# Optimization experiments

Measured on AMD Instinct MI355X. Metric: run time of the kernel, lower is better.

## Reference

```python
import jax, jax.numpy as jnp
import numpy as np

D_MODEL = 1024
NUM_HEADS = 16
DEPTH = D_MODEL // NUM_HEADS


def setup_inputs() -> dict:
    key = jax.random.key(0)
    ks = jax.random.split(key, 9)
    B, S = 2, 2048
    s = 1.0 / np.sqrt(D_MODEL)
    inp = {
        "inputs": jax.random.normal(ks[0], (B, S, D_MODEL), dtype=jnp.float32),
        "wq": jax.random.normal(ks[1], (D_MODEL, D_MODEL), dtype=jnp.float32) * s,
        "bq": jnp.zeros((D_MODEL,), dtype=jnp.float32),
        "wk": jax.random.normal(ks[2], (D_MODEL, D_MODEL), dtype=jnp.float32) * s,
        "bk": jnp.zeros((D_MODEL,), dtype=jnp.float32),
        "wv": jax.random.normal(ks[3], (D_MODEL, D_MODEL), dtype=jnp.float32) * s,
        "bv": jnp.zeros((D_MODEL,), dtype=jnp.float32),
        "wo": jax.random.normal(ks[4], (D_MODEL, D_MODEL), dtype=jnp.float32) * s,
        "bo": jnp.zeros((D_MODEL,), dtype=jnp.float32),
    }
    return inp


def _split_heads(x, B):
    # [B, S, D] -> [B, H, S, depth]
    S = x.shape[1]
    return x.reshape(B, S, NUM_HEADS, DEPTH).transpose(0, 2, 1, 3)


def reference(inputs, wq, bq, wk, bk, wv, bv, wo, bo):
    B, S, _ = inputs.shape
    q = _split_heads(inputs @ wq + bq, B)  # [B,H,S,d]
    k = _split_heads(inputs @ wk + bk, B)
    v = _split_heads(inputs @ wv + bv, B)
    scale = 1.0 / jnp.sqrt(jnp.asarray(DEPTH, dtype=inputs.dtype))
    logits = jnp.einsum("bhqd,bhkd->bhqk", q, k) * scale  # [B,H,S,S]
    attn = jax.nn.softmax(logits, axis=-1)
    out = jnp.einsum("bhqk,bhkd->bhqd", attn, v)  # [B,H,S,d]
    out = out.transpose(0, 2, 1, 3).reshape(B, S, D_MODEL)
    return out @ wo + bo
```

## Files before the change

kernel.cpp:

```cpp
#include <hip/hip_runtime.h>
#include <math.h>

#define SEQ     2048
#define DM      1024
#define NH      16
#define DEPTH   64
#define MTOT    4096

typedef __attribute__((ext_vector_type(8))) _Float16 f16x8;
typedef __attribute__((ext_vector_type(2))) __fp16   fp16v2;
typedef __attribute__((ext_vector_type(4))) float    f32x4;
typedef __attribute__((ext_vector_type(2))) unsigned u32x2;

static __device__ inline unsigned pkh(float a, float b) {
    union { fp16v2 h; unsigned u; } c;
    c.h = __builtin_amdgcn_cvt_pkrtz(a, b);
    return c.u;
}

#define GLOBAL_AS(p) ((const __attribute__((address_space(1))) void*)(p))
#define LDS_AS(p)    ((__attribute__((address_space(3))) void*)(p))

#define K2  0.18033688011112043f
#define C2 -17.31234049066756f
#define EXP2(x) __builtin_amdgcn_exp2f(x)

#define DMA_SRC_C8(lane)  ((((lane) & 3) ^ (((lane) >> 3) & 3)) * 8)
#define FRAG_C8(lx,quad)  ((((quad) ^ (((lx) >> 1) & 3))) * 8)
#define DMA_SRC64(lane)   ((((lane) & 7) ^ (((lane) >> 3) & 7)) * 8)
#define FRAG64(lx,c)      ((((c) ^ ((lx) & 7))) * 8)

__global__ __launch_bounds__(256)
void prep(const float* __restrict__ X,
          const float* __restrict__ w0, const float* __restrict__ w1,
          const float* __restrict__ w2, const float* __restrict__ w3,
          short* __restrict__ Xb,
          short* __restrict__ o0, short* __restrict__ o1,
          short* __restrict__ o2, short* __restrict__ o3) {
    const int t = threadIdx.x;
    const int z = blockIdx.z;
    if (z >= 4) {
        int r0 = (z - 4) * 1024 + blockIdx.x * 64;
        int c0 = blockIdx.y * 64;
        #pragma unroll
        for (int i = 0; i < 4; i++) {
            int row = r0 + i * 16 + (t >> 4);
            int c4  = c0 + (t & 15) * 4;
            float4 v = *(const float4*)&X[(size_t)row * DM + c4];
            u32x2 o; o.x = pkh(v.x, v.y); o.y = pkh(v.z, v.w);
            *(u32x2*)&Xb[(size_t)row * DM + c4] = o;
        }
        return;
    }
    const float* W; short* O;
    switch (z) {
        case 0: W = w0; O = o0; break;
        case 1: W = w1; O = o1; break;
        case 2: W = w2; O = o2; break;
        default: W = w3; O = o3; break;
    }
    __shared__ float Tf[64][65];
    const int k0 = blockIdx.x * 64, n0 = blockIdx.y * 64;
    #pragma unroll
    for (int i = 0; i < 4; i++) {
        int row = i * 16 + (t >> 4);
        int c4  = (t & 15) * 4;
        float4 v = *(const float4*)&W[(size_t)(k0 + row) * DM + n0 + c4];
        Tf[row][c4 + 0] = v.x; Tf[row][c4 + 1] = v.y;
        Tf[row][c4 + 2] = v.z; Tf[row][c4 + 3] = v.w;
    }
    __syncthreads();
    #pragma unroll
    for (int i = 0; i < 4; i++) {
        int nrow = i * 16 + (t >> 4);
        int kc4  = (t & 15) * 4;
        u32x2 o;
        o.x = pkh(Tf[kc4 + 0][nrow], Tf[kc4 + 1][nrow]);
        o.y = pkh(Tf[kc4 + 2][nrow], Tf[kc4 + 3][nrow]);
        *(u32x2*)&O[(size_t)(n0 + nrow) * DM + k0 + kc4] = o;
    }
}

__global__ __launch_bounds__(256)
void gemm_qkv(const short* __restrict__ Xb,
              const short* __restrict__ Wqt, const short* __restrict__ Wkt,
              const short* __restrict__ Wvt,
              const float* __restrict__ bq, const float* __restrict__ bk,
              const float* __restrict__ bv,
              short* __restrict__ Qw, short* __restrict__ Kw,
              short* __restrict__ Vtw) {
    const int z = blockIdx.z;
    const short* A; const short* B; const float* bias;
    if (z == 0)      { A = Xb;  B = Wqt; bias = bq; }
    else if (z == 1) { A = Xb;  B = Wkt; bias = bk; }
    else             { A = Wvt; B = Xb;  bias = bv; }
    const int bx = blockIdx.x;
    int m0, n0;
    if (z < 2) { n0 = (bx & 7) * 128; m0 = (bx >> 3) * 128; }
    else       { m0 = (bx & 7) * 128; n0 = (bx >> 3) * 128; }

    __shared__ short As[128 * 64];
    __shared__ short Bs[128 * 64];
    const int t = threadIdx.x, lane = t & 63, w = t >> 6;
    const int lx = lane & 15, quad = lane >> 4;
    const int wm = (w & 1) * 64, wn = (w >> 1) * 64;
    const int r8 = lane >> 3;
    const int cs = DMA_SRC64(lane);

    f32x4 acc[4][4];
    #pragma unroll
    for (int i = 0; i < 4; i++)
        #pragma unroll
        for (int j = 0; j < 4; j++)
            acc[i][j] = (f32x4){0.f, 0.f, 0.f, 0.f};

    for (int k0 = 0; k0 < DM; k0 += 64) {
        #pragma unroll
        for (int j = 0; j < 4; j++) {
            int rb = w * 32 + j * 8;
            __builtin_amdgcn_global_load_lds(
                GLOBAL_AS(A + (size_t)(m0 + rb + r8) * DM + k0 + cs),
                LDS_AS(As + rb * 64), 16, 0, 0);
            __builtin_amdgcn_global_load_lds(
                GLOBAL_AS(B + (size_t)(n0 + rb + r8) * DM + k0 + cs),
                LDS_AS(Bs + rb * 64), 16, 0, 0);
        }
        __syncthreads();

        #pragma unroll
        for (int ks = 0; ks < 2; ks++) {
            const int fo = FRAG64(lx, ks * 4 + quad);
            f16x8 af[4], bfr[4];
            #pragma unroll
            for (int mt = 0; mt < 4; mt++)
                af[mt] = *(f16x8*)&As[(wm + mt * 16 + lx) * 64 + fo];
            #pragma unroll
            for (int nt = 0; nt < 4; nt++)
                bfr[nt] = *(f16x8*)&Bs[(wn + nt * 16 + lx) * 64 + fo];
            #pragma unroll
            for (int mt = 0; mt < 4; mt++)
                #pragma unroll
                for (int nt = 0; nt < 4; nt++)
                    acc[mt][nt] = __builtin_amdgcn_mfma_f32_16x16x32_f16(
                        af[mt], bfr[nt], acc[mt][nt], 0, 0, 0);
        }
        __syncthreads();
    }

    if (z < 2) {
        short* Cp = (z == 0) ? Qw : Kw;
        float bi[4];
        #pragma unroll
        for (int nt = 0; nt < 4; nt++) bi[nt] = bias[n0 + wn + nt * 16 + lx];
        #pragma unroll
        for (int mt = 0; mt < 4; mt++) {
            #pragma unroll
            for (int reg = 0; reg < 4; reg++) {
                int row = m0 + wm + mt * 16 + quad * 4 + reg;
                u32x2 o;
                o.x = pkh(acc[mt][0][reg] + bi[0], acc[mt][1][reg] + bi[1]);
                o.y = pkh(acc[mt][2][reg] + bi[2], acc[mt][3][reg] + bi[3]);
                *(u32x2*)&Cp[(size_t)row * DM + n0 + wn + 4 * lx] = o;
            }
        }
    } else {
        int colbase = n0 + wn;
        int bsel    = colbase >> 11;
        int kb      = colbase & 2047;
        short* Vbh  = Vtw + (size_t)bsel * ((size_t)NH * DEPTH * SEQ);
        int so = ((lx >> 2) * 8) + ((lx & 3) * 2);
        #pragma unroll
        for (int mt = 0; mt < 4; mt++) {
            #pragma unroll
            for (int reg = 0; reg < 4; reg++) {
                int row = m0 + wm + mt * 16 + quad * 4 + reg;
                float bb = bias[row];
                unsigned w01 = pkh(acc[mt][0][reg] + bb, acc[mt][1][reg] + bb);
                unsigned w23 = pkh(acc[mt][2][reg] + bb, acc[mt][3][reg] + bb);
                *(unsigned*)&Vbh[(size_t)row * SEQ + kb + so]      = w01;
                *(unsigned*)&Vbh[(size_t)row * SEQ + kb + so + 32] = w23;
            }
        }
    }
}

__global__ __launch_bounds__(256)
void gemm_out(const short* __restrict__ A, const short* __restrict__ B,
              const float* __restrict__ bias, float* __restrict__ C) {
    __shared__ short As[128 * 64];
    __shared__ short Bs[64 * 64];
    const int t = threadIdx.x, lane = t & 63, w = t >> 6;
    const int lx = lane & 15, quad = lane >> 4;
    const int n0 = blockIdx.x * 64, m0 = blockIdx.y * 128;
    const int wm = (w & 1) * 64, wn = (w >> 1) * 32;
    const int r8 = lane >> 3;
    const int cs = DMA_SRC64(lane);

    f32x4 acc[4][2];
    #pragma unroll
    for (int i = 0; i < 4; i++)
        #pragma unroll
        for (int j = 0; j < 2; j++)
            acc[i][j] = (f32x4){0.f, 0.f, 0.f, 0.f};

    for (int k0 = 0; k0 < DM; k0 += 64) {
        #pragma unroll
        for (int j = 0; j < 4; j++) {
            int rb = w * 32 + j * 8;
            __builtin_amdgcn_global_load_lds(
                GLOBAL_AS(A + (size_t)(m0 + rb + r8) * DM + k0 + cs),
                LDS_AS(As + rb * 64), 16, 0, 0);
        }
        #pragma unroll
        for (int j = 0; j < 2; j++) {
            int rb = w * 16 + j * 8;
            __builtin_amdgcn_global_load_lds(
                GLOBAL_AS(B + (size_t)(n0 + rb + r8) * DM + k0 + cs),
                LDS_AS(Bs + rb * 64), 16, 0, 0);
        }
        __syncthreads();

        #pragma unroll
        for (int ks = 0; ks < 2; ks++) {
            const int fo = FRAG64(lx, ks * 4 + quad);
            f16x8 af[4], bfr[2];
            #pragma unroll
            for (int mt = 0; mt < 4; mt++)
                af[mt] = *(f16x8*)&As[(wm + mt * 16 + lx) * 64 + fo];
            #pragma unroll
            for (int nt = 0; nt < 2; nt++)
                bfr[nt] = *(f16x8*)&Bs[(wn + nt * 16 + lx) * 64 + fo];
            #pragma unroll
            for (int mt = 0; mt < 4; mt++)
                #pragma unroll
                for (int nt = 0; nt < 2; nt++)
                    acc[mt][nt] = __builtin_amdgcn_mfma_f32_16x16x32_f16(
                        af[mt], bfr[nt], acc[mt][nt], 0, 0, 0);
        }
        __syncthreads();
    }

    #pragma unroll
    for (int mt = 0; mt < 4; mt++)
        #pragma unroll
        for (int nt = 0; nt < 2; nt++)
            #pragma unroll
            for (int reg = 0; reg < 4; reg++) {
                int row = m0 + wm + mt * 16 + quad * 4 + reg;
                int col = n0 + wn + nt * 16 + lx;
                C[(size_t)row * DM + col] = acc[mt][nt][reg] + bias[col];
            }
}

__global__ __launch_bounds__(512)
void flash_mfma(const short* __restrict__ Q, const short* __restrict__ K,
                const short* __restrict__ Vt, short* __restrict__ O) {
    __shared__ short Ks[2][2][128 * 32];
    __shared__ short Vs[2][4][64 * 32];

    const int t = threadIdx.x, lane = t & 63, w = t >> 6;
    const int lx = lane & 15, quad = lane >> 4;
    const int h = blockIdx.y, bb = blockIdx.z;
    const int q0 = blockIdx.x * 128;
    const int r4 = lane >> 2;
    const int cs  = DMA_SRC_C8(lane);
    const int fa  = FRAG_C8(lx, quad);

    f16x8 qa[2];
    #pragma unroll
    for (int ks = 0; ks < 2; ks++)
        qa[ks] = *(const f16x8*)&Q[(size_t)(bb * SEQ + q0 + w * 16 + lx) * DM
                                   + h * DEPTH + ks * 32 + quad * 8];

    f32x4 of[4];
    float l_acc = 0.f;
    #pragma unroll
    for (int dt = 0; dt < 4; dt++) of[dt] = (f32x4){0.f, 0.f, 0.f, 0.f};

    const short* Kb = K  + (size_t)bb * SEQ * DM + h * DEPTH;
    const short* Vb = Vt + (size_t)(bb * NH + h) * DEPTH * SEQ;

    const int kdh = w >> 2;
    const int krg = (w & 3) * 16;
    const int vsh = w & 3;
    const int vdg = (w >> 2) * 16;

    auto stage = [&](int kt, int sb) {
        const int kbase = kt * 128;
        const short* kg = Kb + (size_t)(kbase + krg + r4) * DM + kdh * 32;
        __builtin_amdgcn_global_load_lds(GLOBAL_AS(kg + cs),
            LDS_AS(&Ks[sb][kdh][krg * 32]), 16, 0, 0);
        __builtin_amdgcn_global_load_lds(GLOBAL_AS(kg + (size_t)64 * DM + cs),
            LDS_AS(&Ks[sb][kdh][(krg + 64) * 32]), 16, 0, 0);
        const short* vg = Vb + (size_t)(vdg + r4) * SEQ + kbase + vsh * 32;
        __builtin_amdgcn_global_load_lds(GLOBAL_AS(vg + cs),
            LDS_AS(&Vs[sb][vsh][vdg * 32]), 16, 0, 0);
        __builtin_amdgcn_global_load_lds(GLOBAL_AS(vg + (size_t)32 * SEQ + cs),
            LDS_AS(&Vs[sb][vsh][(vdg + 32) * 32]), 16, 0, 0);
    };

    stage(0, 0);
    __syncthreads();

    int buf = 0;
    for (int kt = 0; kt < SEQ / 128; kt++) {
        if (kt + 1 < SEQ / 128) stage(kt + 1, buf ^ 1);

        f32x4 st[8];
        #pragma unroll
        for (int nt = 0; nt < 8; nt++)
            st[nt] = (f32x4){0.f, 0.f, 0.f, 0.f};
        #pragma unroll
        for (int ks = 0; ks < 2; ks++) {
            #pragma unroll
            for (int g = 0; g < 2; g++) {
                f16x8 kb[4];
                #pragma unroll
                for (int n4 = 0; n4 < 4; n4++)
                    kb[n4] = *(f16x8*)&Ks[buf][ks][((g * 4 + n4) * 16 + lx) * 32 + fa];
                __builtin_amdgcn_s_setprio(1);
                #pragma unroll
                for (int n4 = 0; n4 < 4; n4++)
                    st[g * 4 + n4] = __builtin_amdgcn_mfma_f32_16x16x32_f16(
                        kb[n4], qa[ks], st[g * 4 + n4], 0, 0, 0);
                __builtin_amdgcn_s_setprio(0);
            }
        }

        f16x8 pa[4];
        #pragma unroll
        for (int g = 0; g < 2; g++)
            #pragma unroll
            for (int ks = 0; ks < 2; ks++) {
                union { f16x8 v; unsigned u[4]; } pu;
                #pragma unroll
                for (int wd = 0; wd < 4; wd++) {
                    float pe = EXP2(fmaf(st[g * 4 + 2 * ks + 0][wd], K2, C2));
                    float po = EXP2(fmaf(st[g * 4 + 2 * ks + 1][wd], K2, C2));
                    l_acc += pe + po;
                    pu.u[wd] = pkh(pe, po);
                }
                pa[g * 2 + ks] = pu.v;
            }

        #pragma unroll
        for (int sh = 0; sh < 4; sh++) {
            f16x8 vb[4];
            #pragma unroll
            for (int dt = 0; dt < 4; dt++)
                vb[dt] = *(f16x8*)&Vs[buf][sh][(dt * 16 + lx) * 32 + fa];
            __builtin_amdgcn_s_setprio(1);
            #pragma unroll
            for (int dt = 0; dt < 4; dt++)
                of[dt] = __builtin_amdgcn_mfma_f32_16x16x32_f16(
                    pa[sh], vb[dt], of[dt], 0, 0, 0);
            __builtin_amdgcn_s_setprio(0);
        }

        __syncthreads();
        buf ^= 1;
    }

    _Float16* Oh = (_Float16*)O;
    {
        float l = l_acc;
        l += __shfl_xor(l, 16);
        l += __shfl_xor(l, 32);
        #pragma unroll
        for (int reg = 0; reg < 4; reg++) {
            float lrow = __shfl(l, quad * 4 + reg, 64);
            float inv  = 1.0f / lrow;
            size_t row = (size_t)bb * SEQ + q0 + w * 16 + quad * 4 + reg;
            #pragma unroll
            for (int dt = 0; dt < 4; dt++)
                Oh[row * DM + h * DEPTH + dt * 16 + lx] = (_Float16)(of[dt][reg] * inv);
        }
    }
}

extern "C" void kernel_launch(void* const* d_in, const int* in_sizes, int n_in,
                              void* d_out, int out_size, void* d_ws, size_t ws_size,
                              hipStream_t stream) {
    const float* X  = (const float*)d_in[0];
    const float* wq = (const float*)d_in[1];
    const float* bq = (const float*)d_in[2];
    const float* wk = (const float*)d_in[3];
    const float* bk = (const float*)d_in[4];
    const float* wv = (const float*)d_in[5];
    const float* bv = (const float*)d_in[6];
    const float* wo = (const float*)d_in[7];
    const float* bo = (const float*)d_in[8];
    float* out = (float*)d_out;

    short* Xb  = (short*)d_ws;
    short* Wqt = Xb  + (size_t)MTOT * DM;
    short* Wkt = Wqt + (size_t)DM * DM;
    short* Wvt = Wkt + (size_t)DM * DM;
    short* Wot = Wvt + (size_t)DM * DM;
    short* Qw  = Wot + (size_t)DM * DM;
    short* Kw  = Qw  + (size_t)MTOT * DM;
    short* Vtw = Kw  + (size_t)MTOT * DM;
    short* AO  = Vtw + (size_t)MTOT * DM;

    hipLaunchKernelGGL(prep, dim3(16, 16, 8), dim3(256), 0, stream,
                       X, wq, wk, wv, wo, Xb, Wqt, Wkt, Wvt, Wot);

    hipLaunchKernelGGL(gemm_qkv, dim3(256, 1, 3), dim3(256), 0, stream,
                       Xb, Wqt, Wkt, Wvt, bq, bk, bv, Qw, Kw, Vtw);

    hipLaunchKernelGGL(flash_mfma, dim3(SEQ / 128, NH, 2), dim3(512), 0, stream,
                       Qw, Kw, Vtw, AO);

    hipLaunchKernelGGL(gemm_out, dim3(16, 32), dim3(256), 0, stream,
                       AO, Wot, bo, out);
}
```

Baseline: 195.9 us.

## Double-buffer LDS tiles in QKV and output GEMMs to overlap loads with MFMA

Both projection GEMMs now keep two LDS stages. The next K-slice is issued via global_load_lds before the MFMAs on the current slice, so global-to-LDS transfer latency can hide behind compute and one barrier per iteration is dropped. The MFMA block is also wrapped in s_setprio to raise wave priority during compute. This doubles LDS use per block, which may lower occupancy. Correctness relies on the single end-of-iteration barrier making the async DMA visible before the next iteration reads it.

Result: faster. 191.7 us (-2.2%).

```diff
diff --git a/kernel.cpp b/kernel.cpp
--- a/kernel.cpp
+++ b/kernel.cpp
@@ -99,8 +99,8 @@
     if (z < 2) { n0 = (bx & 7) * 128; m0 = (bx >> 3) * 128; }
     else       { m0 = (bx & 7) * 128; n0 = (bx >> 3) * 128; }
 
-    __shared__ short As[128 * 64];
-    __shared__ short Bs[128 * 64];
+    __shared__ short As[2][128 * 64];
+    __shared__ short Bs[2][128 * 64];
     const int t = threadIdx.x, lane = t & 63, w = t >> 6;
     const int lx = lane & 15, quad = lane >> 4;
     const int wm = (w & 1) * 64, wn = (w >> 1) * 64;
@@ -114,18 +114,26 @@
         for (int j = 0; j < 4; j++)
             acc[i][j] = (f32x4){0.f, 0.f, 0.f, 0.f};
 
-    for (int k0 = 0; k0 < DM; k0 += 64) {
+    auto stage = [&](int kk, int sb) {
+        const int k0 = kk * 64;
         #pragma unroll
         for (int j = 0; j < 4; j++) {
             int rb = w * 32 + j * 8;
             __builtin_amdgcn_global_load_lds(
                 GLOBAL_AS(A + (size_t)(m0 + rb + r8) * DM + k0 + cs),
-                LDS_AS(As + rb * 64), 16, 0, 0);
+                LDS_AS(&As[sb][rb * 64]), 16, 0, 0);
             __builtin_amdgcn_global_load_lds(
                 GLOBAL_AS(B + (size_t)(n0 + rb + r8) * DM + k0 + cs),
-                LDS_AS(Bs + rb * 64), 16, 0, 0);
-        }
-        __syncthreads();
+                LDS_AS(&Bs[sb][rb * 64]), 16, 0, 0);
+        }
+    };
+
+    stage(0, 0);
+    __syncthreads();
+
+    int buf = 0;
+    for (int kk = 0; kk < DM / 64; kk++) {
+        if (kk + 1 < DM / 64) stage(kk + 1, buf ^ 1);
 
         #pragma unroll
         for (int ks = 0; ks < 2; ks++) {
@@ -133,18 +141,22 @@
             f16x8 af[4], bfr[4];
             #pragma unroll
             for (int mt = 0; mt < 4; mt++)
-                af[mt] = *(f16x8*)&As[(wm + mt * 16 + lx) * 64 + fo];
+                af[mt] = *(f16x8*)&As[buf][(wm + mt * 16 + lx) * 64 + fo];
             #pragma unroll
             for (int nt = 0; nt < 4; nt++)
-                bfr[nt] = *(f16x8*)&Bs[(wn + nt * 16 + lx) * 64 + fo];
+                bfr[nt] = *(f16x8*)&Bs[buf][(wn + nt * 16 + lx) * 64 + fo];
+            __builtin_amdgcn_s_setprio(1);
             #pragma unroll
             for (int mt = 0; mt < 4; mt++)
                 #pragma unroll
                 for (int nt = 0; nt < 4; nt++)
                     acc[mt][nt] = __builtin_amdgcn_mfma_f32_16x16x32_f16(
                         af[mt], bfr[nt], acc[mt][nt], 0, 0, 0);
-        }
+            __builtin_amdgcn_s_setprio(0);
+        }
+
         __syncthreads();
+        buf ^= 1;
     }
 
     if (z < 2) {
@@ -187,8 +199,8 @@
 __global__ __launch_bounds__(256)
 void gemm_out(const short* __restrict__ A, const short* __restrict__ B,
               const float* __restrict__ bias, float* __restrict__ C) {
-    __shared__ short As[128 * 64];
-    __shared__ short Bs[64 * 64];
+    __shared__ short As[2][128 * 64];
+    __shared__ short Bs[2][64 * 64];
     const int t = threadIdx.x, lane = t & 63, w = t >> 6;
     const int lx = lane & 15, quad = lane >> 4;
     const int n0 = blockIdx.x * 64, m0 = blockIdx.y * 128;
@@ -203,22 +215,30 @@
         for (int j = 0; j < 2; j++)
             acc[i][j] = (f32x4){0.f, 0.f, 0.f, 0.f};
 
-    for (int k0 = 0; k0 < DM; k0 += 64) {
+    auto stage = [&](int kk, int sb) {
+        const int k0 = kk * 64;
         #pragma unroll
         for (int j = 0; j < 4; j++) {
             int rb = w * 32 + j * 8;
             __builtin_amdgcn_global_load_lds(
                 GLOBAL_AS(A + (size_t)(m0 + rb + r8) * DM + k0 + cs),
-                LDS_AS(As + rb * 64), 16, 0, 0);
+                LDS_AS(&As[sb][rb * 64]), 16, 0, 0);
         }
         #pragma unroll
         for (int j = 0; j < 2; j++) {
             int rb = w * 16 + j * 8;
             __builtin_amdgcn_global_load_lds(
                 GLOBAL_AS(B + (size_t)(n0 + rb + r8) * DM + k0 + cs),
-                LDS_AS(Bs + rb * 64), 16, 0, 0);
-        }
-        __syncthreads();
+                LDS_AS(&Bs[sb][rb * 64]), 16, 0, 0);
+        }
+    };
+
+    stage(0, 0);
+    __syncthreads();
+
+    int buf = 0;
+    for (int kk = 0; kk < DM / 64; kk++) {
+        if (kk + 1 < DM / 64) stage(kk + 1, buf ^ 1);
 
         #pragma unroll
         for (int ks = 0; ks < 2; ks++) {
@@ -226,18 +246,22 @@
             f16x8 af[4], bfr[2];
             #pragma unroll
             for (int mt = 0; mt < 4; mt++)
-                af[mt] = *(f16x8*)&As[(wm + mt * 16 + lx) * 64 + fo];
+                af[mt] = *(f16x8*)&As[buf][(wm + mt * 16 + lx) * 64 + fo];
             #pragma unroll
             for (int nt = 0; nt < 2; nt++)
-                bfr[nt] = *(f16x8*)&Bs[(wn + nt * 16 + lx) * 64 + fo];
+                bfr[nt] = *(f16x8*)&Bs[buf][(wn + nt * 16 + lx) * 64 + fo];
+            __builtin_amdgcn_s_setprio(1);
             #pragma unroll
             for (int mt = 0; mt < 4; mt++)
                 #pragma unroll
                 for (int nt = 0; nt < 2; nt++)
                     acc[mt][nt] = __builtin_amdgcn_mfma_f32_16x16x32_f16(
                         af[mt], bfr[nt], acc[mt][nt], 0, 0, 0);
-        }
+            __builtin_amdgcn_s_setprio(0);
+        }
+
         __syncthreads();
+        buf ^= 1;
     }
 
     #pragma unroll
```
